# Performance work log

Measured on AMD Instinct MI355X. Metric: run time of the kernel, lower is better.

The kernel has to match this reference:

```python
import jax, jax.numpy as jnp
import numpy as np

D = 128  # inputs / head dim

def setup_inputs() -> dict:
    key = jax.random.key(0)
    ks = jax.random.split(key, 7)
    B, S = 4, 4096
    s = 1.0 / np.sqrt(D)
    return {
        "x": jax.random.normal(ks[0], (B, S, D), dtype=jnp.float32),
        "Wq": jax.random.normal(ks[1], (D, D), dtype=jnp.float32) * s,
        "bq": jax.random.normal(ks[2], (D,), dtype=jnp.float32) * s,
        "Wk": jax.random.normal(ks[3], (D, D), dtype=jnp.float32) * s,
        "bk": jax.random.normal(ks[4], (D,), dtype=jnp.float32) * s,
        "Wv": jax.random.normal(ks[5], (D, D), dtype=jnp.float32) * s,
        "bv": jax.random.normal(ks[6], (D,), dtype=jnp.float32) * s,
    }

def reference(x, Wq, bq, Wk, bk, Wv, bv):
    B, S, d = x.shape
    # nn.Linear: y = x @ W^T + b
    q = jnp.einsum('bsd,ed->bse', x, Wq) + bq
    k = jnp.einsum('bsd,ed->bse', x, Wk) + bk
    v = jnp.einsum('bsd,ed->bse', x, Wv) + bv
    scores = jnp.einsum('bse,bte->bst', q, k) / jnp.sqrt(jnp.asarray(d, x.dtype))
    attn = jax.nn.softmax(scores, axis=-1)
    out = jnp.einsum('bst,bte->bse', attn, v)
    return out.reshape(B, S * d)
```

## Files before the change

### kernel.cpp

```cpp
#include <hip/hip_runtime.h>
#include <hip/hip_bf16.h>

typedef __bf16 bf16x8 __attribute__((ext_vector_type(8)));
typedef __bf16 bf16x4 __attribute__((ext_vector_type(4)));
typedef float  f32x4  __attribute__((ext_vector_type(4)));

#define NB 4
#define SEQ 4096
#define DIM 128

static __device__ __forceinline__ unsigned int bf16bits(__bf16 h) {
    return (unsigned int)__builtin_bit_cast(unsigned short, h);
}

__global__ __launch_bounds__(256) void wconv(
    const float* __restrict__ Wq, const float* __restrict__ Wk,
    const float* __restrict__ Wv,
    __bf16* __restrict__ Wh, __bf16* __restrict__ Wl)
{
    int idx = blockIdx.x * 256 + threadIdx.x;
    int which = idx >> 12;
    int off = (idx & 4095) * 4;
    const float* W = which == 0 ? Wq : (which == 1 ? Wk : Wv);
    float4 v = *(const float4*)(W + off);
    bf16x4 h, lo;
    h[0] = (__bf16)v.x; h[1] = (__bf16)v.y; h[2] = (__bf16)v.z; h[3] = (__bf16)v.w;
    lo[0] = (__bf16)(v.x - (float)h[0]);
    lo[1] = (__bf16)(v.y - (float)h[1]);
    lo[2] = (__bf16)(v.z - (float)h[2]);
    lo[3] = (__bf16)(v.w - (float)h[3]);
    *(bf16x4*)(Wh + which * 16384 + off) = h;
    *(bf16x4*)(Wl + which * 16384 + off) = lo;
}

__global__ __launch_bounds__(256) void qkv_proj(
    const float* __restrict__ x,
    const __bf16* __restrict__ Whg, const __bf16* __restrict__ Wlg,
    const float* __restrict__ bq, const float* __restrict__ bk,
    const float* __restrict__ bv,
    __bf16* __restrict__ Q, __bf16* __restrict__ K, __bf16* __restrict__ Vt)
{
    __shared__ __bf16 vbuf[64][136];
    const int t  = threadIdx.x;
    const int w  = t >> 6, l = t & 63, lg = l >> 4, ll = l & 15;
    const int rt = blockIdx.x, which = blockIdx.y;

    const __bf16* Wh = Whg + which * 16384;
    const __bf16* Wl = Wlg + which * 16384;
    const float* bias = which == 0 ? bq : (which == 1 ? bk : bv);

    float bfr[8];
    #pragma unroll
    for (int ct = 0; ct < 8; ++ct) bfr[ct] = bias[ct * 16 + ll];

    f32x4 acc[8];
    #pragma unroll
    for (int ct = 0; ct < 8; ++ct) acc[ct] = (f32x4){0.f, 0.f, 0.f, 0.f};

    const float* xrow = x + (rt * 64 + w * 16 + ll) * 128;

    #pragma unroll 1
    for (int kb = 0; kb < 4; ++kb) {
        float4 xa = *(const float4*)(xrow + kb * 32 + lg * 8);
        float4 xb = *(const float4*)(xrow + kb * 32 + lg * 8 + 4);
        float xv[8] = {xa.x, xa.y, xa.z, xa.w, xb.x, xb.y, xb.z, xb.w};
        bf16x8 xh, xl;
        #pragma unroll
        for (int j = 0; j < 8; ++j) {
            __bf16 h = (__bf16)xv[j];
            xh[j] = h;
            xl[j] = (__bf16)(xv[j] - (float)h);
        }
        #pragma unroll
        for (int ct = 0; ct < 8; ++ct) {
            bf16x8 wh = *(const bf16x8*)(Wh + (ct * 16 + ll) * 128 + kb * 32 + lg * 8);
            bf16x8 wl = *(const bf16x8*)(Wl + (ct * 16 + ll) * 128 + kb * 32 + lg * 8);
            acc[ct] = __builtin_amdgcn_mfma_f32_16x16x32_bf16(xh, wh, acc[ct], 0, 0, 0);
            acc[ct] = __builtin_amdgcn_mfma_f32_16x16x32_bf16(xh, wl, acc[ct], 0, 0, 0);
            acc[ct] = __builtin_amdgcn_mfma_f32_16x16x32_bf16(xl, wh, acc[ct], 0, 0, 0);
        }
    }

    const float qscale = 0.08838834764831845f;
    const float scale = (which == 0) ? qscale : 1.0f;
    #pragma unroll
    for (int ct = 0; ct < 8; ++ct)
        #pragma unroll
        for (int r = 0; r < 4; ++r)
            vbuf[w * 16 + lg * 4 + r][ct * 16 + ll] = (__bf16)((acc[ct][r] + bfr[ct]) * scale);
    __syncthreads();

    if (which < 2) {
        __bf16* dst = (which == 0 ? Q : K) + (rt * 64 + (t >> 2)) * 128 + (t & 3) * 32;
        const __bf16* src = &vbuf[t >> 2][(t & 3) * 32];
        #pragma unroll
        for (int i = 0; i < 4; ++i) ((bf16x8*)dst)[i] = ((const bf16x8*)src)[i];
    } else {
        int e = t >> 1, sh = (t & 1) * 32;
        int bb = rt >> 6, sb = (rt & 63) * 64 + sh;
        __bf16 tmp[32];
        #pragma unroll
        for (int j = 0; j < 32; ++j) tmp[j] = vbuf[sh + j][e];
        __bf16* dst = Vt + bb * (128 * 4096) + e * 4096 + sb;
        #pragma unroll
        for (int i = 0; i < 4; ++i) ((bf16x8*)dst)[i] = *(const bf16x8*)&tmp[i * 8];
    }
}

__global__ __launch_bounds__(512, 2) void attn_fwd(
    const __bf16* __restrict__ Qg,
    const __bf16* __restrict__ Kg,
    const __bf16* __restrict__ Vt,
    float* __restrict__ out)
{
    __shared__ __bf16 Kl[2][64][136];
    __shared__ __bf16 Vl[2][128][72];
    __shared__ __bf16 PlT[8][16][72];
    __shared__ float  Obuf[64][132];
    __shared__ float  m_l[2][64], l_l[2][64];

    const int t  = threadIdx.x;
    const int w  = t >> 6;
    const int g  = w >> 2;
    const int wl = w & 3;
    const int l  = t & 63, lg = l >> 4, ll = l & 15;
    const int tg = t & 255;

    const int bid = blockIdx.x;
    const int b = bid >> 6, qt = bid & 63;
    const int rb = wl * 16;
    const int qrow0 = qt * 64 + rb;

    bf16x8 qa[4];
    const __bf16* qbase = Qg + (b * 4096 + qrow0 + ll) * 128 + lg * 8;
    #pragma unroll
    for (int kb = 0; kb < 4; ++kb) qa[kb] = *(const bf16x8*)(qbase + kb * 32);

    f32x4 o[8];
    #pragma unroll
    for (int dt = 0; dt < 8; ++dt) o[dt] = (f32x4){0.f, 0.f, 0.f, 0.f};
    float m = -1e30f, lsum = 0.f;

    const __bf16* kbase = Kg + (long)(b * 4096 + g * 2048) * 128;
    const __bf16* vbase = Vt + (long)b * 128 * 4096 + g * 2048;

    const int ur[4] = {tg >> 4, (tg + 256) >> 4, (tg + 512) >> 4, (tg + 768) >> 4};
    const int uc[4] = {tg & 15, tg & 15, tg & 15, tg & 15};
    const int vr[4] = {tg >> 3, (tg + 256) >> 3, (tg + 512) >> 3, (tg + 768) >> 3};
    const int vc = tg & 7;

    bf16x8 kreg[4], vreg[4];
    #pragma unroll
    for (int ii = 0; ii < 4; ++ii)
        kreg[ii] = *(const bf16x8*)(kbase + ur[ii] * 128 + uc[ii] * 8);
    #pragma unroll
    for (int ii = 0; ii < 4; ++ii)
        vreg[ii] = *(const bf16x8*)(vbase + vr[ii] * 4096 + vc * 8);
    #pragma unroll
    for (int ii = 0; ii < 4; ++ii) *(bf16x8*)&Kl[g][ur[ii]][uc[ii] * 8] = kreg[ii];
    #pragma unroll
    for (int ii = 0; ii < 4; ++ii) *(bf16x8*)&Vl[g][vr[ii]][vc * 8] = vreg[ii];
    __syncthreads();

    for (int it = 0; it < 32; ++it) {
        if (it + 1 < 32) {
            int kv = (it + 1) * 64;
            #pragma unroll
            for (int ii = 0; ii < 4; ++ii)
                kreg[ii] = *(const bf16x8*)(kbase + (kv + ur[ii]) * 128 + uc[ii] * 8);
            #pragma unroll
            for (int ii = 0; ii < 4; ++ii)
                vreg[ii] = *(const bf16x8*)(vbase + vr[ii] * 4096 + kv + vc * 8);
        }

        float p[4][4];
        #pragma unroll
        for (int nt = 0; nt < 4; ++nt) {
            f32x4 f = (f32x4){0.f, 0.f, 0.f, 0.f};
            #pragma unroll
            for (int kb = 0; kb < 4; ++kb) {
                bf16x8 kf = *(const bf16x8*)&Kl[g][nt * 16 + ll][kb * 32 + lg * 8];
                f = __builtin_amdgcn_mfma_f32_16x16x32_bf16(kf, qa[kb], f, 0, 0, 0);
            }
            #pragma unroll
            for (int r = 0; r < 4; ++r) p[nt][r] = f[r];
        }

        float mx = p[0][0];
        #pragma unroll
        for (int nt = 0; nt < 4; ++nt)
            #pragma unroll
            for (int r = 0; r < 4; ++r) mx = fmaxf(mx, p[nt][r]);
        mx = fmaxf(mx, __shfl_xor(mx, 16, 64));
        mx = fmaxf(mx, __shfl_xor(mx, 32, 64));
        float mnew = fmaxf(m, mx);
        float alpha = __expf(m - mnew);

        float rsum = 0.f;
        unsigned int pk[4][2];
        #pragma unroll
        for (int nt = 0; nt < 4; ++nt) {
            __bf16 pb[4];
            #pragma unroll
            for (int r = 0; r < 4; ++r) {
                float e = __expf(p[nt][r] - mnew);
                pb[r] = (__bf16)e;
                rsum += (float)pb[r];
            }
            pk[nt][0] = bf16bits(pb[0]) | (bf16bits(pb[1]) << 16);
            pk[nt][1] = bf16bits(pb[2]) | (bf16bits(pb[3]) << 16);
        }
        rsum += __shfl_xor(rsum, 16, 64);
        rsum += __shfl_xor(rsum, 32, 64);
        lsum = lsum * alpha + rsum;
        m = mnew;

        #pragma unroll
        for (int nt = 0; nt < 4; ++nt) {
            uint2 u2; u2.x = pk[nt][0]; u2.y = pk[nt][1];
            *(uint2*)&PlT[w][ll][nt * 16 + lg * 4] = u2;
        }
        asm volatile("s_waitcnt lgkmcnt(0)" ::: "memory");
        __builtin_amdgcn_sched_barrier(0);

        float arow[4];
        #pragma unroll
        for (int r = 0; r < 4; ++r) arow[r] = __shfl(alpha, lg * 4 + r, 64);
        #pragma unroll
        for (int dt = 0; dt < 8; ++dt)
            #pragma unroll
            for (int r = 0; r < 4; ++r) o[dt][r] *= arow[r];

        #pragma unroll
        for (int kc = 0; kc < 2; ++kc) {
            bf16x8 pa = *(const bf16x8*)&PlT[w][ll][kc * 32 + lg * 8];
            #pragma unroll
            for (int dt = 0; dt < 8; ++dt) {
                bf16x8 vb = *(const bf16x8*)&Vl[g][dt * 16 + ll][kc * 32 + lg * 8];
                o[dt] = __builtin_amdgcn_mfma_f32_16x16x32_bf16(pa, vb, o[dt], 0, 0, 0);
            }
        }

        __syncthreads();
        if (it + 1 < 32) {
            #pragma unroll
            for (int ii = 0; ii < 4; ++ii) *(bf16x8*)&Kl[g][ur[ii]][uc[ii] * 8] = kreg[ii];
            #pragma unroll
            for (int ii = 0; ii < 4; ++ii) *(bf16x8*)&Vl[g][vr[ii]][vc * 8] = vreg[ii];
        }
        __syncthreads();
    }

    if (lg == 0) { m_l[g][rb + ll] = m; l_l[g][rb + ll] = lsum; }
    __syncthreads();

    float a_own[4], inv[4];
    #pragma unroll
    for (int r = 0; r < 4; ++r) {
        int qr = rb + lg * 4 + r;
        float m0 = m_l[0][qr], m1 = m_l[1][qr];
        float l0 = l_l[0][qr], l1 = l_l[1][qr];
        float mst = fmaxf(m0, m1);
        float a0 = __expf(m0 - mst), a1 = __expf(m1 - mst);
        float lst = l0 * a0 + l1 * a1;
        a_own[r] = (g == 0) ? a0 : a1;
        inv[r] = 1.f / lst;
    }
    if (g == 1) {
        #pragma unroll
        for (int dt = 0; dt < 8; ++dt)
            #pragma unroll
            for (int r = 0; r < 4; ++r)
                Obuf[rb + lg * 4 + r][dt * 16 + ll] = o[dt][r] * a_own[r];
    }
    __syncthreads();
    if (g == 0) {
        float* ob = out + (long)(b * 4096 + qt * 64) * 128;
        #pragma unroll
        for (int r = 0; r < 4; ++r) {
            int qr = rb + lg * 4 + r;
            #pragma unroll
            for (int dt = 0; dt < 8; ++dt)
                ob[qr * 128 + dt * 16 + ll] =
                    (o[dt][r] * a_own[r] + Obuf[qr][dt * 16 + ll]) * inv[r];
        }
    }
}

extern "C" void kernel_launch(void* const* d_in, const int* in_sizes, int n_in,
                              void* d_out, int out_size, void* d_ws, size_t ws_size,
                              hipStream_t stream) {
    (void)in_sizes; (void)n_in; (void)out_size; (void)ws_size;
    const float* x  = (const float*)d_in[0];
    const float* Wq = (const float*)d_in[1];
    const float* bq = (const float*)d_in[2];
    const float* Wk = (const float*)d_in[3];
    const float* bk = (const float*)d_in[4];
    const float* Wv = (const float*)d_in[5];
    const float* bv = (const float*)d_in[6];
    float* out = (float*)d_out;

    __bf16* Q  = (__bf16*)d_ws;
    __bf16* K  = Q + NB * SEQ * DIM;
    __bf16* Vt = K + NB * SEQ * DIM;
    __bf16* Wh = Vt + NB * SEQ * DIM;
    __bf16* Wl = Wh + 3 * DIM * DIM;

    wconv<<<48, 256, 0, stream>>>(Wq, Wk, Wv, Wh, Wl);
    dim3 g1(256, 3), b1(256);
    qkv_proj<<<g1, b1, 0, stream>>>(x, Wh, Wl, bq, bk, bv, Q, K, Vt);
    attn_fwd<<<256, 512, 0, stream>>>(Q, K, Vt, out);
}
```

Measured before the change: 109.1 us.

## Double-buffer K/V in LDS with swizzle and lazy softmax rescaling

Splits the K/V shared tiles into two ping-pong buffers so the next tile can be stored before the single barrier, dropping one __syncthreads per iteration. Padding is replaced by an XOR swizzle to avoid bank conflicts, and the output/statistics buffers are unioned with the tiles to limit LDS. The softmax skips max updates and output rescaling unless some row's max grows by more than 8, which cuts per-iteration VALU work. In exchange it uses more LDS, and unnormalized exponentials can grow up to e^8.

Result: slower. 207.8 us (+90.5%).

```diff
diff --git a/kernel.cpp b/kernel.cpp
--- a/kernel.cpp
+++ b/kernel.cpp
@@ -107,17 +107,24 @@
     }
 }
 
+struct ShA {
+    __bf16 Kl[2][2][64][128];
+    __bf16 Vl[2][2][128][64];
+    __bf16 PlT[8][16][72];
+};
+struct ShB {
+    float Obuf[64][132];
+    float m_l[2][64], l_l[2][64];
+};
+union ShU { ShA a; ShB b; };
+
 __global__ __launch_bounds__(512, 2) void attn_fwd(
     const __bf16* __restrict__ Qg,
     const __bf16* __restrict__ Kg,
     const __bf16* __restrict__ Vt,
     float* __restrict__ out)
 {
-    __shared__ __bf16 Kl[2][64][136];
-    __shared__ __bf16 Vl[2][128][72];
-    __shared__ __bf16 PlT[8][16][72];
-    __shared__ float  Obuf[64][132];
-    __shared__ float  m_l[2][64], l_l[2][64];
+    __shared__ ShU sh;
 
     const int t  = threadIdx.x;
     const int w  = t >> 6;
@@ -125,6 +132,7 @@
     const int wl = w & 3;
     const int l  = t & 63, lg = l >> 4, ll = l & 15;
     const int tg = t & 255;
+    const int sK = ll & 7;
 
     const int bid = blockIdx.x;
     const int b = bid >> 6, qt = bid & 63;
@@ -144,57 +152,75 @@
     const __bf16* kbase = Kg + (long)(b * 4096 + g * 2048) * 128;
     const __bf16* vbase = Vt + (long)b * 128 * 4096 + g * 2048;
 
-    const int ur[4] = {tg >> 4, (tg + 256) >> 4, (tg + 512) >> 4, (tg + 768) >> 4};
-    const int uc[4] = {tg & 15, tg & 15, tg & 15, tg & 15};
-    const int vr[4] = {tg >> 3, (tg + 256) >> 3, (tg + 512) >> 3, (tg + 768) >> 3};
-    const int vc = tg & 7;
+    int krow[4], kuc[4], kswz[4], vrow[4], vuc[4], vswz[4];
+    #pragma unroll
+    for (int ii = 0; ii < 4; ++ii) {
+        int u = tg + ii * 256;
+        krow[ii] = u >> 4; kuc[ii] = u & 15; kswz[ii] = kuc[ii] ^ (krow[ii] & 7);
+        vrow[ii] = u >> 3; vuc[ii] = u & 7;  vswz[ii] = vuc[ii] ^ (vrow[ii] & 7);
+    }
 
     bf16x8 kreg[4], vreg[4];
     #pragma unroll
     for (int ii = 0; ii < 4; ++ii)
-        kreg[ii] = *(const bf16x8*)(kbase + ur[ii] * 128 + uc[ii] * 8);
+        kreg[ii] = *(const bf16x8*)(kbase + krow[ii] * 128 + kuc[ii] * 8);
     #pragma unroll
     for (int ii = 0; ii < 4; ++ii)
-        vreg[ii] = *(const bf16x8*)(vbase + vr[ii] * 4096 + vc * 8);
-    #pragma unroll
-    for (int ii = 0; ii < 4; ++ii) *(bf16x8*)&Kl[g][ur[ii]][uc[ii] * 8] = kreg[ii];
-    #pragma unroll
-    for (int ii = 0; ii < 4; ++ii) *(bf16x8*)&Vl[g][vr[ii]][vc * 8] = vreg[ii];
+        vreg[ii] = *(const bf16x8*)(vbase + vrow[ii] * 4096 + vuc[ii] * 8);
+    #pragma unroll
+    for (int ii = 0; ii < 4; ++ii)
+        *(bf16x8*)&sh.a.Kl[g][0][krow[ii]][kswz[ii] * 8] = kreg[ii];
+    #pragma unroll
+    for (int ii = 0; ii < 4; ++ii)
+        *(bf16x8*)&sh.a.Vl[g][0][vrow[ii]][vswz[ii] * 8] = vreg[ii];
     __syncthreads();
 
+    int p = 0;
     for (int it = 0; it < 32; ++it) {
         if (it + 1 < 32) {
             int kv = (it + 1) * 64;
             #pragma unroll
             for (int ii = 0; ii < 4; ++ii)
-                kreg[ii] = *(const bf16x8*)(kbase + (kv + ur[ii]) * 128 + uc[ii] * 8);
+                kreg[ii] = *(const bf16x8*)(kbase + (kv + krow[ii]) * 128 + kuc[ii] * 8);
             #pragma unroll
             for (int ii = 0; ii < 4; ++ii)
-                vreg[ii] = *(const bf16x8*)(vbase + vr[ii] * 4096 + kv + vc * 8);
-        }
-
-        float p[4][4];
+                vreg[ii] = *(const bf16x8*)(vbase + vrow[ii] * 4096 + kv + vuc[ii] * 8);
+        }
+
+        float sc[4][4];
         #pragma unroll
         for (int nt = 0; nt < 4; ++nt) {
             f32x4 f = (f32x4){0.f, 0.f, 0.f, 0.f};
             #pragma unroll
             for (int kb = 0; kb < 4; ++kb) {
-                bf16x8 kf = *(const bf16x8*)&Kl[g][nt * 16 + ll][kb * 32 + lg * 8];
+                bf16x8 kf = *(const bf16x8*)&sh.a.Kl[g][p][nt * 16 + ll][((kb * 4 + lg) ^ sK) * 8];
                 f = __builtin_amdgcn_mfma_f32_16x16x32_bf16(kf, qa[kb], f, 0, 0, 0);
             }
             #pragma unroll
-            for (int r = 0; r < 4; ++r) p[nt][r] = f[r];
-        }
-
-        float mx = p[0][0];
+            for (int r = 0; r < 4; ++r) sc[nt][r] = f[r];
+        }
+
+        float mx = sc[0][0];
         #pragma unroll
         for (int nt = 0; nt < 4; ++nt)
             #pragma unroll
-            for (int r = 0; r < 4; ++r) mx = fmaxf(mx, p[nt][r]);
+            for (int r = 0; r < 4; ++r) mx = fmaxf(mx, sc[nt][r]);
         mx = fmaxf(mx, __shfl_xor(mx, 16, 64));
         mx = fmaxf(mx, __shfl_xor(mx, 32, 64));
-        float mnew = fmaxf(m, mx);
-        float alpha = __expf(m - mnew);
+
+        if (__any(mx - m > 8.f)) {
+            float mnew = fmaxf(m, mx);
+            float alpha = __expf(m - mnew);
+            float arow[4];
+            #pragma unroll
+            for (int r = 0; r < 4; ++r) arow[r] = __shfl(alpha, lg * 4 + r, 64);
+            #pragma unroll
+            for (int dt = 0; dt < 8; ++dt)
+                #pragma unroll
+                for (int r = 0; r < 4; ++r) o[dt][r] *= arow[r];
+            lsum *= alpha;
+            m = mnew;
+        }
 
         float rsum = 0.f;
         unsigned int pk[4][2];
@@ -203,7 +229,7 @@
             __bf16 pb[4];
             #pragma unroll
             for (int r = 0; r < 4; ++r) {
-                float e = __expf(p[nt][r] - mnew);
+                float e = __expf(sc[nt][r] - m);
                 pb[r] = (__bf16)e;
                 rsum += (float)pb[r];
             }
@@ -212,54 +238,47 @@
         }
         rsum += __shfl_xor(rsum, 16, 64);
         rsum += __shfl_xor(rsum, 32, 64);
-        lsum = lsum * alpha + rsum;
-        m = mnew;
+        lsum += rsum;
 
         #pragma unroll
         for (int nt = 0; nt < 4; ++nt) {
             uint2 u2; u2.x = pk[nt][0]; u2.y = pk[nt][1];
-            *(uint2*)&PlT[w][ll][nt * 16 + lg * 4] = u2;
+            *(uint2*)&sh.a.PlT[w][ll][nt * 16 + lg * 4] = u2;
         }
         asm volatile("s_waitcnt lgkmcnt(0)" ::: "memory");
         __builtin_amdgcn_sched_barrier(0);
 
-        float arow[4];
-        #pragma unroll
-        for (int r = 0; r < 4; ++r) arow[r] = __shfl(alpha, lg * 4 + r, 64);
-        #pragma unroll
-        for (int dt = 0; dt < 8; ++dt)
-            #pragma unroll
-            for (int r = 0; r < 4; ++r) o[dt][r] *= arow[r];
-
         #pragma unroll
         for (int kc = 0; kc < 2; ++kc) {
-            bf16x8 pa = *(const bf16x8*)&PlT[w][ll][kc * 32 + lg * 8];
+            bf16x8 pa = *(const bf16x8*)&sh.a.PlT[w][ll][kc * 32 + lg * 8];
             #pragma unroll
             for (int dt = 0; dt < 8; ++dt) {
-                bf16x8 vb = *(const bf16x8*)&Vl[g][dt * 16 + ll][kc * 32 + lg * 8];
+                bf16x8 vb = *(const bf16x8*)&sh.a.Vl[g][p][dt * 16 + ll][((kc * 4 + lg) ^ sK) * 8];
                 o[dt] = __builtin_amdgcn_mfma_f32_16x16x32_bf16(pa, vb, o[dt], 0, 0, 0);
             }
         }
 
+        if (it + 1 < 32) {
+            #pragma unroll
+            for (int ii = 0; ii < 4; ++ii)
+                *(bf16x8*)&sh.a.Kl[g][p ^ 1][krow[ii]][kswz[ii] * 8] = kreg[ii];
+            #pragma unroll
+            for (int ii = 0; ii < 4; ++ii)
+                *(bf16x8*)&sh.a.Vl[g][p ^ 1][vrow[ii]][vswz[ii] * 8] = vreg[ii];
+        }
         __syncthreads();
-        if (it + 1 < 32) {
-            #pragma unroll
-            for (int ii = 0; ii < 4; ++ii) *(bf16x8*)&Kl[g][ur[ii]][uc[ii] * 8] = kreg[ii];
-            #pragma unroll
-            for (int ii = 0; ii < 4; ++ii) *(bf16x8*)&Vl[g][vr[ii]][vc * 8] = vreg[ii];
-        }
-        __syncthreads();
-    }
-
-    if (lg == 0) { m_l[g][rb + ll] = m; l_l[g][rb + ll] = lsum; }
+        p ^= 1;
+    }
+
+    if (lg == 0) { sh.b.m_l[g][rb + ll] = m; sh.b.l_l[g][rb + ll] = lsum; }
     __syncthreads();
 
     float a_own[4], inv[4];
     #pragma unroll
     for (int r = 0; r < 4; ++r) {
         int qr = rb + lg * 4 + r;
-        float m0 = m_l[0][qr], m1 = m_l[1][qr];
-        float l0 = l_l[0][qr], l1 = l_l[1][qr];
+        float m0 = sh.b.m_l[0][qr], m1 = sh.b.m_l[1][qr];
+        float l0 = sh.b.l_l[0][qr], l1 = sh.b.l_l[1][qr];
         float mst = fmaxf(m0, m1);
         float a0 = __expf(m0 - mst), a1 = __expf(m1 - mst);
         float lst = l0 * a0 + l1 * a1;
@@ -271,7 +290,7 @@
         for (int dt = 0; dt < 8; ++dt)
             #pragma unroll
             for (int r = 0; r < 4; ++r)
-                Obuf[rb + lg * 4 + r][dt * 16 + ll] = o[dt][r] * a_own[r];
+                sh.b.Obuf[rb + lg * 4 + r][dt * 16 + ll] = o[dt][r] * a_own[r];
     }
     __syncthreads();
     if (g == 0) {
@@ -282,7 +301,7 @@
             #pragma unroll
             for (int dt = 0; dt < 8; ++dt)
                 ob[qr * 128 + dt * 16 + ll] =
-                    (o[dt][r] * a_own[r] + Obuf[qr][dt * 16 + ll]) * inv[r];
+                    (o[dt][r] * a_own[r] + sh.b.Obuf[qr][dt * 16 + ll]) * inv[r];
         }
     }
 }
```
